# Performance work log

Hardware: AMD Instinct MI355X
Metric: run time of the kernel (lower is better)

## Reference

```python
import jax, jax.numpy as jnp
from jax import lax
import numpy as np

ANCHOR_LENGTHS = (2.0, 4.0, 6.0, 9.0, 13.0, 18.0)  # A = 6


def make_anchors_1d(Lf, anchor_lengths):
    # anchors on the feature axis: [Lf*A, 2] (start, end)
    al = jnp.asarray(anchor_lengths, dtype=jnp.float32)          # [A]
    centers = jnp.arange(Lf, dtype=jnp.float32) + 0.5            # [Lf]
    start = centers[:, None] - 0.5 * al[None, :]                 # [Lf, A]
    end = centers[:, None] + 0.5 * al[None, :]                   # [Lf, A]
    return jnp.stack([start, end], axis=-1).reshape(Lf * al.shape[0], 2)


def setup_inputs() -> dict:
    key = jax.random.key(0)
    ks = jax.random.split(key, 4)
    B, C, Lf, A = 4, 512, 8192, len(ANCHOR_LENGTHS)
    feat = jax.random.normal(ks[0], (B, C, Lf), dtype=jnp.float32)
    conv_w = jax.random.normal(ks[1], (C, C, 3), dtype=jnp.float32) * 0.02   # OIW
    conv_b = jnp.zeros((C,), dtype=jnp.float32)
    obj_w = jax.random.normal(ks[2], (A, C, 1), dtype=jnp.float32) * 0.02
    obj_b = jnp.zeros((A,), dtype=jnp.float32)
    reg_w = jax.random.normal(ks[3], (A * 2, C, 1), dtype=jnp.float32) * 0.02
    reg_b = jnp.zeros((A * 2,), dtype=jnp.float32)
    return {"feat": feat, "conv_w": conv_w, "conv_b": conv_b,
            "obj_w": obj_w, "obj_b": obj_b, "reg_w": reg_w, "reg_b": reg_b}


def reference(feat, conv_w, conv_b, obj_w, obj_b, reg_w, reg_b):
    B, C, Lf = feat.shape
    A = obj_w.shape[0]
    # 3x1 conv, padding=1 -> SAME; layout N C W / O I W
    h = lax.conv_general_dilated(feat, conv_w, window_strides=(1,),
                                 padding="SAME",
                                 dimension_numbers=("NCH", "OIH", "NCH"))
    h = jax.nn.relu(h + conv_b[None, :, None])                   # [B, C, Lf]
    # 1x1 conv heads expressed as channel contractions
    obj = jnp.einsum("bcl,ac->bal", h, obj_w[:, :, 0]) + obj_b[None, :, None]   # [B, A, Lf]
    reg = jnp.einsum("bcl,ac->bal", h, reg_w[:, :, 0]) + reg_b[None, :, None]   # [B, 2A, Lf]
    obj = obj.transpose(0, 2, 1).reshape(B, Lf * A)                              # [B, N]
    reg = reg.transpose(0, 2, 1).reshape(B, Lf, A, 2).reshape(B, Lf * A, 2)      # [B, N, 2]
    anchors = make_anchors_1d(Lf, ANCHOR_LENGTHS)                                # [N, 2]
    return obj, reg, anchors
```

## Files before the change

### kernel.cpp

```cpp
#include <hip/hip_runtime.h>
#include <stdint.h>

typedef __attribute__((ext_vector_type(8))) short short8;
typedef __attribute__((ext_vector_type(4))) float f32x4;
typedef __attribute__((ext_vector_type(4))) float float4v;
typedef __attribute__((ext_vector_type(4))) unsigned short u16x4;
typedef __attribute__((ext_vector_type(8))) unsigned short u16x8;

#define AS1 __attribute__((address_space(1)))
#define AS3 __attribute__((address_space(3)))


__device__ __forceinline__ unsigned short f2bf(float f) {
    union { float f; unsigned int u; } v; v.f = f;
    unsigned int r = v.u + 0x7fffu + ((v.u >> 16) & 1u);
    return (unsigned short)(r >> 16);
}

__constant__ float c_AL[6] = {2.f, 4.f, 6.f, 9.f, 13.f, 18.f};

__global__ __launch_bounds__(256) void prep_kernel(
    const float* __restrict__ conv_w, const float* __restrict__ obj_w,
    const float* __restrict__ reg_w, unsigned short* __restrict__ wAf,
    unsigned short* __restrict__ hwp, unsigned short* __restrict__ featT,
    float* __restrict__ out) {
    unsigned int idx = blockIdx.x * 256 + threadIdx.x;
    if (idx < 786432u) {
        unsigned int chunkid = idx >> 9;
        unsigned int within = idx & 511u;
        unsigned int lane = within >> 3, j = within & 7u;
        unsigned int kc = chunkid & 15u;
        unsigned int ct = chunkid >> 4;
        unsigned int t = ct % 3u, cb = ct / 3u;
        unsigned int cout = cb * 16u + (lane & 15u);
        unsigned int cin = kc * 32u + (lane >> 4) * 8u + j;
        wAf[idx] = f2bf(conv_w[(cout * 512u + cin) * 3u + t]);
    } else if (idx < 802816u) {
        unsigned int i2 = idx - 786432u;
        unsigned int j = i2 >> 9, c = i2 & 511u;
        float v = 0.f;
        if (j < 6u) v = obj_w[j * 512u + c];
        else if (j < 18u) v = reg_w[(j - 6u) * 512u + c];
        hwp[i2] = f2bf(v);
    } else if (idx < 851968u) {
        unsigned int n = idx - 802816u;
        unsigned int l = n / 6u, a = n - l * 6u;
        float ctr = (float)l + 0.5f, half = 0.5f * c_AL[a];
        float* anchors = out + 589824;
        anchors[2 * n]     = ctr - half;
        anchors[2 * n + 1] = ctr + half;
    } else if (idx < 856064u) {
        unsigned int i4 = idx - 851968u;
        unsigned int b = i4 >> 10, rem = i4 & 1023u;
        unsigned int row = (rem >> 9) ? 8193u : 0u;
        unsigned int c = rem & 511u;
        featT[((size_t)b * 8208 + row) * 512 + c] = 0;
    }
}

__global__ __launch_bounds__(256) void transpose_kernel(
    const float* __restrict__ feat, unsigned short* __restrict__ featT) {
    __shared__ unsigned short tile[64][68];
    int tid = threadIdx.x;
    int l0 = blockIdx.x * 64, c0 = blockIdx.y * 64, b = blockIdx.z;
    const float* fb = feat + ((size_t)b * 512 + c0) * 8192 + l0;
    #pragma unroll
    for (int it = 0; it < 4; ++it) {
        int slot = it * 256 + tid;
        int c = slot >> 4, l4 = (slot & 15) << 2;
        float4v v = *(const float4v*)(fb + (size_t)c * 8192 + l4);
        u16x4 pk;
        pk.x = f2bf(v.x); pk.y = f2bf(v.y);
        pk.z = f2bf(v.z); pk.w = f2bf(v.w);
        *(u16x4*)(&tile[c][l4]) = pk;
    }
    __syncthreads();
    unsigned short* ftb = featT + ((size_t)b * 8208 + 1 + l0) * 512 + c0;
    #pragma unroll
    for (int it = 0; it < 2; ++it) {
        int slot = it * 256 + tid;
        int l = slot >> 3, c8 = (slot & 7) << 3;
        u16x8 pk;
        #pragma unroll
        for (int j = 0; j < 8; ++j) pk[j] = tile[c8 + j][l];
        *(u16x8*)(ftb + (size_t)l * 512 + c8) = pk;
    }
}

__global__ __launch_bounds__(256, 3) void conv_gemm_kernel(
    const unsigned short* __restrict__ wAf,
    const unsigned short* __restrict__ featT,
    const float* __restrict__ conv_b,
    const unsigned short* __restrict__ hwp,
    float* __restrict__ part) {
    __shared__ unsigned short smem[17408];

    const int tid = threadIdx.x;
    const int wave = tid >> 6, lane = tid & 63;
    const int lq = lane >> 4, lr = lane & 15;
    const int l0 = blockIdx.x * 128;
    const int m0 = blockIdx.y * 128;
    const int b = blockIdx.z;
    const int wm = wave >> 1, wn = wave & 1;
    const unsigned short* ftb = featT + (size_t)b * 8208 * 512;

    f32x4 acc[4][4];
    #pragma unroll
    for (int i = 0; i < 4; ++i)
        #pragma unroll
        for (int j = 0; j < 4; ++j)
            acc[i][j] = (f32x4){0.f, 0.f, 0.f, 0.f};

    for (int kc = 0; kc < 16; ++kc) {
        __syncthreads();
        for (int ci = wave; ci < 9; ci += 4) {
            const unsigned short* g =
                ftb + (size_t)(l0 + ci * 16 + lr) * 512 + kc * 32 + lq * 8;
            __builtin_amdgcn_global_load_lds((const AS1 void*)g,
                                             (AS3 void*)(smem + ci * 512), 16, 0, 0);
        }
        short8 af[3][4];
        #pragma unroll
        for (int t = 0; t < 3; ++t)
            #pragma unroll
            for (int fm = 0; fm < 4; ++fm)
                af[t][fm] = *(const short8*)(
                    wAf + ((size_t)(((m0 >> 4) + wm * 4 + fm) * 3 + t) * 16 + kc) * 512 + lane * 8);
        __syncthreads();
        #pragma unroll
        for (int t = 0; t < 3; ++t) {
            short8 bf[4];
            #pragma unroll
            for (int fn = 0; fn < 4; ++fn) {
                int R = wn * 64 + fn * 16 + lr + t;
                bf[fn] = *(const short8*)(smem + ((R >> 4) << 9) +
                                          ((((lq << 4) | (R & 15))) << 3));
            }
            #pragma unroll
            for (int fm = 0; fm < 4; ++fm)
                #pragma unroll
                for (int fn = 0; fn < 4; ++fn)
                    acc[fm][fn] = __builtin_amdgcn_mfma_f32_16x16x32_bf16(
                        af[t][fm], bf[fn], acc[fm][fn], 0, 0, 0);
        }
    }
    __syncthreads();
    #pragma unroll
    for (int fm = 0; fm < 4; ++fm) {
        int mb = wm * 64 + fm * 16 + lq * 4;
        float cb0 = conv_b[m0 + mb];
        float cb1 = conv_b[m0 + mb + 1];
        float cb2 = conv_b[m0 + mb + 2];
        float cb3 = conv_b[m0 + mb + 3];
        #pragma unroll
        for (int fn = 0; fn < 4; ++fn) {
            int n = wn * 64 + fn * 16 + lr;
            f32x4 v = acc[fm][fn];
            u16x4 pk;
            pk.x = f2bf(fmaxf(v.x + cb0, 0.f));
            pk.y = f2bf(fmaxf(v.y + cb1, 0.f));
            pk.z = f2bf(fmaxf(v.z + cb2, 0.f));
            pk.w = f2bf(fmaxf(v.w + cb3, 0.f));
            *(u16x4*)(smem + n * 136 + mb) = pk;
        }
    }
    __syncthreads();
    f32x4 hacc[2][2];
    #pragma unroll
    for (int i = 0; i < 2; ++i) {
        hacc[i][0] = (f32x4){0.f, 0.f, 0.f, 0.f};
        hacc[i][1] = (f32x4){0.f, 0.f, 0.f, 0.f};
    }
    const int lbase = wave * 32;
    for (int kk = 0; kk < 4; ++kk) {
        short8 ha[2], hb2[2];
        #pragma unroll
        for (int fm2 = 0; fm2 < 2; ++fm2)
            ha[fm2] = *(const short8*)(smem + (lbase + fm2 * 16 + lr) * 136 + kk * 32 + lq * 8);
        #pragma unroll
        for (int fn = 0; fn < 2; ++fn)
            hb2[fn] = *(const short8*)(hwp + (size_t)(fn * 16 + lr) * 512 + m0 + kk * 32 + lq * 8);
        #pragma unroll
        for (int fm2 = 0; fm2 < 2; ++fm2)
            #pragma unroll
            for (int fn = 0; fn < 2; ++fn)
                hacc[fm2][fn] = __builtin_amdgcn_mfma_f32_16x16x32_bf16(
                    ha[fm2], hb2[fn], hacc[fm2][fn], 0, 0, 0);
    }
    float* pb = part + ((size_t)(blockIdx.y * 4 + b) * 8192) * 18;
    #pragma unroll
    for (int fn = 0; fn < 2; ++fn) {
        int j = fn * 16 + lr;
        if (j >= 18) continue;
        #pragma unroll
        for (int fm2 = 0; fm2 < 2; ++fm2)
            #pragma unroll
            for (int r = 0; r < 4; ++r) {
                int l = l0 + lbase + fm2 * 16 + lq * 4 + r;
                pb[(size_t)l * 18 + j] = hacc[fm2][fn][r];
            }
    }
}

__global__ __launch_bounds__(256) void reduce_kernel(
    const float* __restrict__ part, const float* __restrict__ obj_b,
    const float* __restrict__ reg_b, float* __restrict__ out) {
    unsigned int idx = blockIdx.x * 256 + threadIdx.x;
    if (idx >= 589824u) return;
    unsigned int j = idx % 18u;
    unsigned int t = idx / 18u;
    unsigned int l = t & 8191u;
    unsigned int b = t >> 13;
    float s = 0.f;
    #pragma unroll
    for (int mb = 0; mb < 4; ++mb)
        s += part[((size_t)(mb * 4 + b) * 8192 + l) * 18 + j];
    if (j < 6u) {
        s += obj_b[j];
        out[(size_t)b * 49152 + l * 6 + j] = s;
    } else {
        s += reg_b[j - 6u];
        out[196608u + (size_t)b * 98304 + l * 12 + (j - 6u)] = s;
    }
}

extern "C" void kernel_launch(void* const* d_in, const int* in_sizes, int n_in,
                              void* d_out, int out_size, void* d_ws, size_t ws_size,
                              hipStream_t stream) {
    const float* feat   = (const float*)d_in[0];
    const float* conv_w = (const float*)d_in[1];
    const float* conv_b = (const float*)d_in[2];
    const float* obj_w  = (const float*)d_in[3];
    const float* obj_b  = (const float*)d_in[4];
    const float* reg_w  = (const float*)d_in[5];
    const float* reg_b  = (const float*)d_in[6];
    float* out = (float*)d_out;
    char* ws = (char*)d_ws;
    unsigned short* wAf   = (unsigned short*)(ws);
    unsigned short* hwp   = (unsigned short*)(ws + 1572864);
    unsigned short* featT = (unsigned short*)(ws + 1605632);
    float* part           = (float*)(ws + 35225600);

    prep_kernel<<<dim3(3344), dim3(256), 0, stream>>>(conv_w, obj_w, reg_w,
                                                      wAf, hwp, featT, out);
    transpose_kernel<<<dim3(128, 8, 4), dim3(256), 0, stream>>>(feat, featT);
    conv_gemm_kernel<<<dim3(64, 4, 4), dim3(256), 0, stream>>>(wAf, featT, conv_b, hwp, part);
    reduce_kernel<<<dim3(2304), dim3(256), 0, stream>>>(part, obj_b, reg_b, out);
}
```

Baseline: 174.6 us.

## Stage conv weights through LDS and merge prep with transpose kernel

The GEMM kernel now copies the weight fragments for all three taps into shared memory with global_load_lds, next to the feature tile, instead of each wave loading them straight into registers. This cuts register pressure, and launch bounds rise from 3 to 4 blocks per CU. Separately, the prep and transpose kernels are fused into one launch to save a kernel launch. The risks are heavier LDS traffic and lost overlap, because the weight loads now sit behind the same barrier as the feature loads.

```diff
diff --git a/kernel.cpp b/kernel.cpp
--- a/kernel.cpp
+++ b/kernel.cpp
@@ -19,12 +19,41 @@
 
 __constant__ float c_AL[6] = {2.f, 4.f, 6.f, 9.f, 13.f, 18.f};
 
-__global__ __launch_bounds__(256) void prep_kernel(
-    const float* __restrict__ conv_w, const float* __restrict__ obj_w,
-    const float* __restrict__ reg_w, unsigned short* __restrict__ wAf,
-    unsigned short* __restrict__ hwp, unsigned short* __restrict__ featT,
-    float* __restrict__ out) {
-    unsigned int idx = blockIdx.x * 256 + threadIdx.x;
+__global__ __launch_bounds__(256) void prep_transpose_kernel(
+    const float* __restrict__ feat, const float* __restrict__ conv_w,
+    const float* __restrict__ obj_w, const float* __restrict__ reg_w,
+    unsigned short* __restrict__ wAf, unsigned short* __restrict__ hwp,
+    unsigned short* __restrict__ featT, float* __restrict__ out) {
+    __shared__ unsigned short tile[64][68];
+    unsigned int bx = blockIdx.x;
+    int tid = threadIdx.x;
+    if (bx < 4096u) {
+        int l0 = (bx & 127) * 64, c0 = ((bx >> 7) & 7) * 64, b = bx >> 10;
+        const float* fb = feat + ((size_t)b * 512 + c0) * 8192 + l0;
+        #pragma unroll
+        for (int it = 0; it < 4; ++it) {
+            int slot = it * 256 + tid;
+            int c = slot >> 4, l4 = (slot & 15) << 2;
+            float4v v = *(const float4v*)(fb + (size_t)c * 8192 + l4);
+            u16x4 pk;
+            pk.x = f2bf(v.x); pk.y = f2bf(v.y);
+            pk.z = f2bf(v.z); pk.w = f2bf(v.w);
+            *(u16x4*)(&tile[c][l4]) = pk;
+        }
+        __syncthreads();
+        unsigned short* ftb = featT + ((size_t)b * 8208 + 1 + l0) * 512 + c0;
+        #pragma unroll
+        for (int it = 0; it < 2; ++it) {
+            int slot = it * 256 + tid;
+            int l = slot >> 3, c8 = (slot & 7) << 3;
+            u16x8 pk;
+            #pragma unroll
+            for (int j = 0; j < 8; ++j) pk[j] = tile[c8 + j][l];
+            *(u16x8*)(ftb + (size_t)l * 512 + c8) = pk;
+        }
+        return;
+    }
+    unsigned int idx = (bx - 4096u) * 256 + tid;
     if (idx < 786432u) {
         unsigned int chunkid = idx >> 9;
         unsigned int within = idx & 511u;
@@ -58,36 +87,7 @@
     }
 }
 
-__global__ __launch_bounds__(256) void transpose_kernel(
-    const float* __restrict__ feat, unsigned short* __restrict__ featT) {
-    __shared__ unsigned short tile[64][68];
-    int tid = threadIdx.x;
-    int l0 = blockIdx.x * 64, c0 = blockIdx.y * 64, b = blockIdx.z;
-    const float* fb = feat + ((size_t)b * 512 + c0) * 8192 + l0;
-    #pragma unroll
-    for (int it = 0; it < 4; ++it) {
-        int slot = it * 256 + tid;
-        int c = slot >> 4, l4 = (slot & 15) << 2;
-        float4v v = *(const float4v*)(fb + (size_t)c * 8192 + l4);
-        u16x4 pk;
-        pk.x = f2bf(v.x); pk.y = f2bf(v.y);
-        pk.z = f2bf(v.z); pk.w = f2bf(v.w);
-        *(u16x4*)(&tile[c][l4]) = pk;
-    }
-    __syncthreads();
-    unsigned short* ftb = featT + ((size_t)b * 8208 + 1 + l0) * 512 + c0;
-    #pragma unroll
-    for (int it = 0; it < 2; ++it) {
-        int slot = it * 256 + tid;
-        int l = slot >> 3, c8 = (slot & 7) << 3;
-        u16x8 pk;
-        #pragma unroll
-        for (int j = 0; j < 8; ++j) pk[j] = tile[c8 + j][l];
-        *(u16x8*)(ftb + (size_t)l * 512 + c8) = pk;
-    }
-}
-
-__global__ __launch_bounds__(256, 3) void conv_gemm_kernel(
+__global__ __launch_bounds__(256, 4) void conv_gemm_kernel(
     const unsigned short* __restrict__ wAf,
     const unsigned short* __restrict__ featT,
     const float* __restrict__ conv_b,
@@ -113,27 +113,29 @@
 
     for (int kc = 0; kc < 16; ++kc) {
         __syncthreads();
-        for (int ci = wave; ci < 9; ci += 4) {
-            const unsigned short* g =
-                ftb + (size_t)(l0 + ci * 16 + lr) * 512 + kc * 32 + lq * 8;
+        for (int ci = wave; ci < 33; ci += 4) {
+            const unsigned short* g;
+            if (ci < 24) {
+                int t = ci >> 3, rb = ci & 7;
+                g = wAf + ((size_t)(((m0 >> 4) + rb) * 3 + t) * 16 + kc) * 512 + lane * 8;
+            } else {
+                int lb = ci - 24;
+                g = ftb + (size_t)(l0 + lb * 16 + lr) * 512 + kc * 32 + lq * 8;
+            }
             __builtin_amdgcn_global_load_lds((const AS1 void*)g,
                                              (AS3 void*)(smem + ci * 512), 16, 0, 0);
         }
-        short8 af[3][4];
-        #pragma unroll
-        for (int t = 0; t < 3; ++t)
+        __syncthreads();
+        #pragma unroll
+        for (int t = 0; t < 3; ++t) {
+            short8 af[4], bf[4];
             #pragma unroll
             for (int fm = 0; fm < 4; ++fm)
-                af[t][fm] = *(const short8*)(
-                    wAf + ((size_t)(((m0 >> 4) + wm * 4 + fm) * 3 + t) * 16 + kc) * 512 + lane * 8);
-        __syncthreads();
-        #pragma unroll
-        for (int t = 0; t < 3; ++t) {
-            short8 bf[4];
+                af[fm] = *(const short8*)(smem + ((t * 8 + wm * 4 + fm) << 9) + (lane << 3));
             #pragma unroll
             for (int fn = 0; fn < 4; ++fn) {
                 int R = wn * 64 + fn * 16 + lr + t;
-                bf[fn] = *(const short8*)(smem + ((R >> 4) << 9) +
+                bf[fn] = *(const short8*)(smem + ((24 + (R >> 4)) << 9) +
                                           ((((lq << 4) | (R & 15))) << 3));
             }
             #pragma unroll
@@ -141,7 +143,7 @@
                 #pragma unroll
                 for (int fn = 0; fn < 4; ++fn)
                     acc[fm][fn] = __builtin_amdgcn_mfma_f32_16x16x32_bf16(
-                        af[t][fm], bf[fn], acc[fm][fn], 0, 0, 0);
+                        af[fm], bf[fn], acc[fm][fn], 0, 0, 0);
         }
     }
     __syncthreads();
@@ -241,9 +243,8 @@
     unsigned short* featT = (unsigned short*)(ws + 1605632);
     float* part           = (float*)(ws + 35225600);
 
-    prep_kernel<<<dim3(3344), dim3(256), 0, stream>>>(conv_w, obj_w, reg_w,
-                                                      wAf, hwp, featT, out);
-    transpose_kernel<<<dim3(128, 8, 4), dim3(256), 0, stream>>>(feat, featT);
+    prep_transpose_kernel<<<dim3(7440), dim3(256), 0, stream>>>(
+        feat, conv_w, obj_w, reg_w, wAf, hwp, featT, out);
     conv_gemm_kernel<<<dim3(64, 4, 4), dim3(256), 0, stream>>>(wAf, featT, conv_b, hwp, part);
     reduce_kernel<<<dim3(2304), dim3(256), 0, stream>>>(part, obj_b, reg_b, out);
 }
```

Result: faster. 166.8 us (-4.5%).
